# Kernel optimization log

Measured on AMD Instinct MI355X. Metric: run time of the kernel, lower is better.

The kernel has to match this reference:

```python
import jax, jax.numpy as jnp
import numpy as np

B, C, H, W = 64, 2048, 18, 9
INF = 1e9  # larger than any |cost| here (costs are -cosine sims in [-1,1])


def hungarian(cost):
    """Exact O(n^3) Jonker-Volgenant assignment (minimize total cost).
    cost: [n, n] float. Returns int32 [n]: column assigned to each row.
    Matches scipy.optimize.linear_sum_assignment on a square matrix.
    Uses 1-based indexing with a virtual row/column 0 (e-maxx formulation)."""
    n = cost.shape[0]
    costp = jnp.zeros((n + 1, n + 1), cost.dtype).at[1:, 1:].set(cost)
    jr = jnp.arange(n + 1)

    def assign_row(i, carry):
        u, v, p = carry          # u,v: dual potentials; p[j] = row matched to col j
        p = p.at[0].set(i)
        way0 = jnp.zeros(n + 1, jnp.int32)
        minv0 = jnp.full(n + 1, INF, cost.dtype)
        used0 = jnp.zeros(n + 1, bool)

        def cond(st):
            return ~st[6]

        def body(st):
            u, v, way, minv, used, j0, done = st
            used = used.at[j0].set(True)
            i0 = p[j0]
            cur = costp[i0] - u[i0] - v                  # reduced costs of row i0, vectorized over cols
            valid = (~used) & (jr >= 1)
            better = valid & (cur < minv)
            minv = jnp.where(better, cur, minv)
            way = jnp.where(better, j0, way)
            mv = jnp.where(valid, minv, INF)
            j1 = jnp.argmin(mv).astype(jnp.int32)
            delta = mv[j1]
            add = jnp.where(used, delta, jnp.zeros((), cost.dtype))
            u = u.at[p].add(add)                          # used cols have distinct p; unused add 0
            v = v - add
            minv = jnp.where(used, minv, minv - delta)
            return u, v, way, minv, used, j1, p[j1] == 0

        u, v, way, _, _, j0, _ = jax.lax.while_loop(
            cond, body, (u, v, way0, minv0, used0, jnp.int32(0), jnp.array(False)))

        def body2(st):
            j0, p = st
            j1 = way[j0]
            return j1, p.at[j0].set(p[j1])

        _, p = jax.lax.while_loop(lambda st: st[0] != 0, body2, (j0, p))
        return u, v, p

    u = jnp.zeros(n + 1, cost.dtype)
    v = jnp.zeros(n + 1, cost.dtype)
    p = jnp.zeros(n + 1, jnp.int32)
    u, v, p = jax.lax.fori_loop(1, n + 1, assign_row, (u, v, p))
    rowcol = jnp.zeros(n + 1, jnp.int32).at[p[1:]].set(jnp.arange(1, n + 1, dtype=jnp.int32))
    return rowcol[1:] - 1


def compute_mask(feat):
    b, c, h, w = feat.shape
    norms = jnp.linalg.norm(feat, axis=1).reshape(b, h * w)
    norms = norms - norms.min(axis=-1, keepdims=True)
    norms = norms / (norms.max(axis=-1, keepdims=True) + 1e-12)
    return jax.lax.stop_gradient(norms.reshape(b, 1, h, w))


def feature_similarity(fq, fk):
    b, c, h, w = fq.shape
    fq = fq.reshape(b, c, h * w)
    fk = fk.reshape(b, c, h * w)
    # F.normalize(dim=1): x / max(||x||, eps)
    nq = fq / jnp.maximum(jnp.linalg.norm(fq, axis=1, keepdims=True), 1e-12)
    nk = fk / jnp.maximum(jnp.linalg.norm(fk, axis=1, keepdims=True), 1e-12)
    return jnp.einsum('bcn,bcm->bnm', nq, nk)  # [b, n, n]


def setup_inputs() -> dict:
    key = jax.random.key(0)
    k1, k2, k3 = jax.random.split(key, 3)
    feat2d = jax.random.normal(k1, (B, C, H, W), dtype=jnp.float32)
    pos_ind = jax.random.randint(k2, (B,), 0, B, dtype=jnp.int64 if jax.config.jax_enable_x64 else jnp.int32).astype(jnp.int32)
    neg_ind = jax.random.randint(k3, (B,), 0, B, dtype=jnp.int32)
    return {"feat2d": feat2d, "pos_ind": pos_ind, "neg_ind": neg_ind}


def reference(feat2d, pos_ind, neg_ind):
    b, c, h, w = feat2d.shape
    n = h * w
    p = n // 2
    mask = compute_mask(feat2d)                         # [b,1,h,w], detached
    maskTr = mask.reshape(b, 1, n)
    s = jnp.sort(maskTr, axis=2)
    thr = s[:, :, p:p + 1]
    bMask = jnp.where(maskTr < thr, 0.0, 1.0).reshape(mask.shape)  # keep top half
    featMasked = feat2d * jax.lax.stop_gradient(bMask)
    featPos = feat2d[pos_ind]
    simPos = feature_similarity(featMasked, featPos)    # [b, n, n]
    # scipy linear_sum_assignment(sim, maximize=True) == minimize(-sim); indices are constants
    cols = jax.vmap(hungarian)(jax.lax.stop_gradient(-simPos))     # [b, n]
    assigned = jnp.take_along_axis(simPos, cols[:, :, None], axis=2)[..., 0]  # [b, n]
    pos_dis = 1.0 - assigned.sum(axis=-1) / p
    return jnp.mean(pos_dis)
```

## Files before the change

### kernel.cpp

```cpp
#include <hip/hip_runtime.h>
#include <hip/hip_bf16.h>

#define Bn 64
#define Cn 2048
#define Nn 162
#define Pn 81
#define NP 176
#define INFV 1.0e9f
#define BIGI 0x7FFFFFFF
#define RBW 328
#define ARRCAP 700

#define OFF_T    0
#define OFF_P    11534336
#define OFF_QS   (OFF_P + 64*32*192)
#define OFF_KS   (OFF_QS + 64*162)
#define OFF_COST (OFF_KS + 64*162)
#define OFF_PD   (OFF_COST + 64*162*162)

typedef __attribute__((ext_vector_type(8))) short bf16x8;
typedef __attribute__((ext_vector_type(4))) float f32x4;
typedef __attribute__((ext_vector_type(4))) unsigned u32x4;

static __device__ __forceinline__ unsigned short f2bf(float x) {
    unsigned int u = __builtin_bit_cast(unsigned int, x);
    unsigned int r = (u + 0x7fffu + ((u >> 16) & 1u)) >> 16;
    return (unsigned short)r;
}
static __device__ __forceinline__ unsigned short f2h(float x) {
    _Float16 h = (_Float16)x;
    return __builtin_bit_cast(unsigned short, h);
}
static __device__ __forceinline__ float h2f(unsigned short u) {
    return (float)__builtin_bit_cast(_Float16, u);
}
static __device__ __forceinline__ unsigned umin32(unsigned a, unsigned b) { return a < b ? a : b; }
static __device__ __forceinline__ unsigned umax32(unsigned a, unsigned b) { return a > b ? a : b; }
static __device__ __forceinline__ unsigned packnn(float v, int id) {
    float c = fmaxf(v, 0.f);
    return (__builtin_bit_cast(unsigned, c) & 0xFFFFFF00u) | (unsigned)id;
}
static __device__ __forceinline__ float unpacknn(unsigned pk) {
    return __builtin_bit_cast(float, pk & 0xFFFFFF00u);
}
static __device__ __forceinline__ unsigned reduceMin64(unsigned x) {
    int v = (int)x, t;
    t = __builtin_amdgcn_update_dpp(0, v, 0x121, 0xF, 0xF, true); v = (int)umin32((unsigned)v, (unsigned)t);
    t = __builtin_amdgcn_update_dpp(0, v, 0x122, 0xF, 0xF, true); v = (int)umin32((unsigned)v, (unsigned)t);
    t = __builtin_amdgcn_update_dpp(0, v, 0x124, 0xF, 0xF, true); v = (int)umin32((unsigned)v, (unsigned)t);
    t = __builtin_amdgcn_update_dpp(0, v, 0x128, 0xF, 0xF, true); v = (int)umin32((unsigned)v, (unsigned)t);
    unsigned a = (unsigned)__builtin_amdgcn_readlane(v, 0);
    unsigned b = (unsigned)__builtin_amdgcn_readlane(v, 16);
    unsigned c = (unsigned)__builtin_amdgcn_readlane(v, 32);
    unsigned d = (unsigned)__builtin_amdgcn_readlane(v, 48);
    return umin32(umin32(a, b), umin32(c, d));
}
static __device__ __forceinline__ int rlanei(int v, int l) { return __builtin_amdgcn_readlane(v, l); }
static __device__ __forceinline__ float rlanef(float v, int l) {
    return __builtin_bit_cast(float, __builtin_amdgcn_readlane(__builtin_bit_cast(int, v), l));
}
static __device__ __forceinline__ int laneOf(int id) { return id < 128 ? (id >> 1) : (id - 128); }
static __device__ __forceinline__ int slotOf(int id) { return id < 128 ? (id & 1) : 2; }
static __device__ __forceinline__ unsigned long long mask_n(int n) {
    if (n <= 0) return 0ull;
    if (n >= 64) return ~0ull;
    return (1ull << n) - 1ull;
}
#define SEL3(s, a0, a1, a2) ((s) == 0 ? (a0) : ((s) == 1 ? (a1) : (a2)))

__global__ __launch_bounds__(256) void k_tr(const float* __restrict__ feat, float* __restrict__ ws) {
    int x = blockIdx.x;
    int cc = x / 3, ct = x % 3;
    int b = blockIdx.y;
    int tid = threadIdx.x;
    int c2 = tid & 31, pg = tid >> 5;
    __shared__ unsigned Tp[32][65];
    __shared__ float Pp[8][64];
    int gc0 = ct * 64 + 2 * c2;
    bool ok  = (gc0 < Nn);
    bool ok1 = (gc0 + 1 < Nn);
    int gcs = ok ? gc0 : 0;
    const float* fb = feat + ((size_t)b * Cn + (size_t)cc * 64) * Nn;
    float2 fa[4], fc[4];
    #pragma unroll
    for (int it = 0; it < 4; ++it) {
        int p = pg + it * 8;
        fa[it] = *(const float2*)(fb + (size_t)(2 * p) * Nn + gcs);
        fc[it] = *(const float2*)(fb + (size_t)(2 * p + 1) * Nn + gcs);
    }
    float s0 = 0.f, s1 = 0.f;
    #pragma unroll
    for (int it = 0; it < 4; ++it) {
        int p = pg + it * 8;
        float ax = ok  ? fa[it].x : 0.f;
        float ay = ok1 ? fa[it].y : 0.f;
        float cx = ok  ? fc[it].x : 0.f;
        float cy = ok1 ? fc[it].y : 0.f;
        s0 = fmaf(ax, ax, fmaf(cx, cx, s0));
        s1 = fmaf(ay, ay, fmaf(cy, cy, s1));
        Tp[p][2 * c2]     = (unsigned)f2bf(ax) | ((unsigned)f2bf(cx) << 16);
        Tp[p][2 * c2 + 1] = (unsigned)f2bf(ay) | ((unsigned)f2bf(cy) << 16);
    }
    Pp[pg][2 * c2]     = s0;
    Pp[pg][2 * c2 + 1] = s1;
    __syncthreads();
    if (tid < 64) {
        float t = 0.f;
        #pragma unroll
        for (int g = 0; g < 8; ++g) t += Pp[g][tid];
        ws[OFF_P + ((size_t)b * 32 + cc) * 192 + ct * 64 + tid] = t;
    }
    unsigned* ft = (unsigned*)(ws + OFF_T);
    size_t base = ((size_t)(b * 32 + cc) * NP + ct * 64) * 32;
    #pragma unroll
    for (int it = 0; it < 8; ++it) {
        int idx = it * 256 + tid;
        int c = idx >> 5;
        int gcol = ct * 64 + c;
        if (gcol < NP) ft[base + idx] = Tp[idx & 31][c];
    }
}

__global__ __launch_bounds__(256) void k_mm(const int* __restrict__ pos_ind,
                                            float* __restrict__ ws) {
    int wg = blockIdx.x;
    int xcd = wg & 7, kk = wg >> 3;
    int b  = xcd + 8 * (kk / 6);
    int mt = kk % 6;
    int tid = threadIdx.x;
    int lane = tid & 63, w = tid >> 6;
    int q0 = mt * 32;
    int pb = pos_ind[b];
    const u32x4* At = (const u32x4*)((const unsigned short*)(ws + OFF_T) + (size_t)b  * NP * Cn);
    const u32x4* Bt = (const u32x4*)((const unsigned short*)(ws + OFF_T) + (size_t)pb * NP * Cn);
    __shared__ u32x4 As[32 * 16];
    __shared__ u32x4 Bs[176 * 16];

    f32x4 a00 = {0.f, 0.f, 0.f, 0.f}, a01 = a00, a02 = a00, a10 = a00, a11 = a00, a12 = a00;
    const int ct0 = w * 3, ct1 = w * 3 + 1, ct2 = w * 3 + 2;
    const bool has2 = (ct2 < 11);
    const int fr = lane & 15, fq = lane >> 4;

    for (int c0 = 0; c0 < Cn; c0 += 128) {
        int cc0 = c0 >> 6;
        #pragma unroll
        for (int it = 0; it < 2; ++it) {
            int task = it * 256 + tid;
            int r = task >> 4, g = task & 15;
            int rowc = q0 + r; if (rowc > NP - 1) rowc = NP - 1;
            As[r * 16 + (g ^ (r & 15))] = At[((size_t)(cc0 + (g >> 3)) * NP + rowc) * 8 + (g & 7)];
        }
        #pragma unroll
        for (int it = 0; it < 11; ++it) {
            int task = it * 256 + tid;
            int col = task >> 4, g = task & 15;
            Bs[col * 16 + (g ^ (col & 15))] = Bt[((size_t)(cc0 + (g >> 3)) * NP + col) * 8 + (g & 7)];
        }
        __syncthreads();
        #pragma unroll
        for (int ks = 0; ks < 4; ++ks) {
            int gk = ks * 4 + fq;
            bf16x8 af0 = *(const bf16x8*)&As[fr * 16 + (gk ^ fr)];
            bf16x8 af1 = *(const bf16x8*)&As[(16 + fr) * 16 + (gk ^ fr)];
            bf16x8 b0 = *(const bf16x8*)&Bs[(ct0 * 16 + fr) * 16 + (gk ^ fr)];
            bf16x8 b1 = *(const bf16x8*)&Bs[(ct1 * 16 + fr) * 16 + (gk ^ fr)];
            a00 = __builtin_amdgcn_mfma_f32_16x16x32_bf16(af0, b0, a00, 0, 0, 0);
            a01 = __builtin_amdgcn_mfma_f32_16x16x32_bf16(af0, b1, a01, 0, 0, 0);
            a10 = __builtin_amdgcn_mfma_f32_16x16x32_bf16(af1, b0, a10, 0, 0, 0);
            a11 = __builtin_amdgcn_mfma_f32_16x16x32_bf16(af1, b1, a11, 0, 0, 0);
            if (has2) {
                bf16x8 b2 = *(const bf16x8*)&Bs[(ct2 * 16 + fr) * 16 + (gk ^ fr)];
                a02 = __builtin_amdgcn_mfma_f32_16x16x32_bf16(af0, b2, a02, 0, 0, 0);
                a12 = __builtin_amdgcn_mfma_f32_16x16x32_bf16(af1, b2, a12, 0, 0, 0);
            }
        }
        __syncthreads();
    }

    float* simg = ws + OFF_COST + (size_t)b * Nn * Nn;
    int c0_ = ct0 * 16 + fr, c1_ = ct1 * 16 + fr, c2_ = ct2 * 16 + fr;
    #pragma unroll
    for (int j = 0; j < 4; ++j) {
        int r0 = q0 + fq * 4 + j;
        int r1 = r0 + 16;
        if (r0 < Nn) {
            if (c0_ < Nn) simg[(size_t)r0 * Nn + c0_] = a00[j];
            if (c1_ < Nn) simg[(size_t)r0 * Nn + c1_] = a01[j];
            if (has2 && c2_ < Nn) simg[(size_t)r0 * Nn + c2_] = a02[j];
        }
        if (r1 < Nn) {
            if (c0_ < Nn) simg[(size_t)r1 * Nn + c0_] = a10[j];
            if (c1_ < Nn) simg[(size_t)r1 * Nn + c1_] = a11[j];
            if (has2 && c2_ < Nn) simg[(size_t)r1 * Nn + c2_] = a12[j];
        }
    }
}

__global__ __launch_bounds__(256) void k_hung(float* __restrict__ ws) {
    const int b = blockIdx.x;
    const int tid = threadIdx.x;
    const int lane = tid & 63, wv = tid >> 6;
    __shared__ unsigned short Cw[(Nn * RBW) / 2 + 32];
    __shared__ int rowBest[Nn + 1];
    __shared__ float Ulds[Nn + 1];
    __shared__ float dvA[192];
    __shared__ float pcm[4][192];
    __shared__ int   pim[4][192];
    __shared__ short rowIdxL[Nn];
    __shared__ float qsL[192];
    __shared__ float ksL[192];
    const float* cg = ws + OFF_COST + (size_t)b * Nn * Nn;

    const bool v2ok = (lane < Nn - 128);
    const int id0 = 2 * lane, id1 = 2 * lane + 1, id2 = 128 + lane;
    const int a32 = 4 * lane;
    const int a16 = 256 + 2 * lane;

    if (tid <= Nn) { rowBest[tid] = BIGI; Ulds[tid] = 0.f; }
    if (tid < 192) dvA[tid] = 0.f;

    float* arrS = &pcm[0][0];
    float* thrP = &pcm[1][0];
    float normv = 0.f, mvalv = 0.f;
    if (tid < Nn) {
        float s = 0.f;
        #pragma unroll
        for (int ch = 0; ch < 32; ++ch) s += ws[OFF_P + ((size_t)b * 32 + ch) * 192 + tid];
        normv = sqrtf(s);
        arrS[tid] = normv;
    }
    __syncthreads();
    {
        float mn = INFV, mx = -INFV;
        for (int k = 0; k < Nn; ++k) { float v = arrS[k]; mn = fminf(mn, v); mx = fmaxf(mx, v); }
        if (tid < Nn) mvalv = (normv - mn) / (mx - mn + 1e-12f);
    }
    __syncthreads();
    if (tid < Nn) arrS[tid] = mvalv;
    __syncthreads();
    if (tid < Nn) {
        int cl = 0, ce = 0, ceb = 0;
        for (int k = 0; k < Nn; ++k) {
            float v = arrS[k];
            cl  += (v <  mvalv);
            ce  += (v == mvalv);
            ceb += (v == mvalv && k < tid);
        }
        if (cl <= Pn && (cl + ce) > Pn && ceb == 0) thrP[0] = mvalv;
    }
    if (tid < 192) { qsL[tid] = 0.f; ksL[tid] = 0.f; }
    __syncthreads();
    if (tid < Nn) {
        float inv = 1.f / fmaxf(normv, 1e-12f);
        ksL[tid] = inv;
        qsL[tid] = (mvalv < thrP[0]) ? 0.f : inv;
    }
    __syncthreads();

    const float ks0f = ksL[id0];
    const float ks1f = ksL[id1];
    const float ks2f = v2ok ? ksL[id2] : 0.f;

    float aq0 = qsL[lane];
    float aq1 = qsL[64 + lane];
    float aq2 = v2ok ? qsL[128 + lane] : 0.f;
    unsigned long long act0 = __ballot(aq0 != 0.f);
    unsigned long long act1 = __ballot(aq1 != 0.f);
    unsigned long long act2 = __ballot(v2ok && aq2 != 0.f);
    int n0 = __popcll(act0), n1 = __popcll(act1), n2 = __popcll(act2);
    const int nact = n0 + n1 + n2;
    if (nact == 0) { if (tid == 0) ws[OFF_PD + b] = 1.f; return; }

    if (wv == 0) {
        unsigned long long lt = (1ull << lane) - 1;
        if ((act0 >> lane) & 1) rowIdxL[__popcll(act0 & lt)] = (short)lane;
        if ((act1 >> lane) & 1) rowIdxL[n0 + __popcll(act1 & lt)] = (short)(64 + lane);
        if (v2ok && ((act2 >> lane) & 1)) rowIdxL[n0 + n1 + __popcll(act2 & lt)] = (short)(128 + lane);
    }
    __syncthreads();

    for (int k = wv; k < nact; k += 4) {
        int orig = rowIdxL[k];
        float qsr = qsL[orig];
        float2 f2 = *(const float2*)(cg + (size_t)orig * Nn + 2 * lane);
        unsigned pk = (unsigned)f2h(-(f2.x * qsr * ks0f))
                    | ((unsigned)f2h(-(f2.y * qsr * ks1f)) << 16);
        *(unsigned*)((char*)Cw + k * RBW + a32) = pk;
        if (v2ok) *(unsigned short*)((char*)Cw + k * RBW + a16) =
            f2h(-(cg[(size_t)orig * Nn + 128 + lane] * qsr * ks2f));
    }
    __syncthreads();

    float cm0 = INFV, cm1 = INFV, cm2 = INFV; int im0 = 0, im1 = 0, im2 = 0;
    for (int k = wv; k < nact; k += 4) {
        unsigned pr = *(const unsigned*)((const char*)Cw + k * RBW + a32);
        float c0 = h2f((unsigned short)pr);
        float c1 = h2f((unsigned short)(pr >> 16));
        float c2 = h2f(*(const unsigned short*)((const char*)Cw + k * RBW + a16));
        if (c0 < cm0) { cm0 = c0; im0 = k + 1; }
        if (c1 < cm1) { cm1 = c1; im1 = k + 1; }
        if (v2ok && c2 < cm2) { cm2 = c2; im2 = k + 1; }
    }
    pcm[wv][id0] = cm0; pim[wv][id0] = im0;
    pcm[wv][id1] = cm1; pim[wv][id1] = im1;
    if (v2ok) { pcm[wv][id2] = cm2; pim[wv][id2] = im2; }
    __syncthreads();

    cm0 = INFV; im0 = 0; cm1 = INFV; im1 = 0; cm2 = INFV; im2 = 0;
    #pragma unroll
    for (int ww = 0; ww < 4; ++ww) {
        float c; int im;
        c = pcm[ww][id0]; im = pim[ww][id0];
        if (im > 0 && (im0 == 0 || c < cm0 || (c == cm0 && im < im0))) { cm0 = c; im0 = im; }
        c = pcm[ww][id1]; im = pim[ww][id1];
        if (im > 0 && (im1 == 0 || c < cm1 || (c == cm1 && im < im1))) { cm1 = c; im1 = im; }
        if (v2ok) {
            c = pcm[ww][id2]; im = pim[ww][id2];
            if (im > 0 && (im2 == 0 || c < cm2 || (c == cm2 && im < im2))) { cm2 = c; im2 = im; }
        }
    }
    if (wv == 0) {
        if (im0 > 0) atomicMin(&rowBest[im0], id0);
        if (im1 > 0) atomicMin(&rowBest[im1], id1);
        if (v2ok && im2 > 0) atomicMin(&rowBest[im2], id2);
    }
    __syncthreads();

    float v0 = cm0, v1 = cm1, v2 = v2ok ? cm2 : 0.f;
    int Pa0 = (im0 > 0 && rowBest[im0] == id0) ? im0 : 0;
    int Pa1 = (im1 > 0 && rowBest[im1] == id1) ? im1 : 0;
    int Pa2 = (v2ok && im2 > 0 && rowBest[im2] == id2) ? im2 : 0;

    unsigned long long cb0 = __ballot(lane + 1 <= nact && rowBest[lane + 1] != BIGI);
    unsigned long long cb1 = __ballot(lane + 65 <= nact && rowBest[lane + 65] != BIGI);
    unsigned long long cb2 = __ballot(lane + 129 <= nact && rowBest[lane + 129] != BIGI);
    unsigned long long fr0 = mask_n(nact)       & ~cb0;
    unsigned long long fr1 = mask_n(nact - 64)  & ~cb1;
    unsigned long long fr2 = mask_n(nact - 128) & ~cb2;

    for (int k = wv; k < nact; k += 4) {
        int j1c = rowBest[k + 1];
        if (j1c == BIGI) continue;
        int roff = k * RBW;
        unsigned pr = *(const unsigned*)((const char*)Cw + roff + a32);
        float r0 = h2f((unsigned short)pr) - v0;
        float r1 = h2f((unsigned short)(pr >> 16)) - v1;
        float r2 = h2f(*(const unsigned short*)((const char*)Cw + roff + a16)) - v2;
        unsigned p0 = (id0 == j1c) ? 0xFFFFFFFFu : packnn(r0, id0);
        unsigned p1 = (id1 == j1c) ? 0xFFFFFFFFu : packnn(r1, id1);
        unsigned p2 = (v2ok && id2 != j1c) ? packnn(r2, id2) : 0xFFFFFFFFu;
        unsigned pk = reduceMin64(umin32(p0, umin32(p1, p2)));
        float min2 = unpacknn(pk);
        if (lane == 0) { dvA[j1c] = min2; Ulds[k + 1] = min2; }
    }
    __syncthreads();
    if (wv != 0) return;

    float ur0, ur1, ur2;
    v0 -= dvA[id0]; ur0 = dvA[id0];
    v1 -= dvA[id1]; ur1 = dvA[id1];
    if (v2ok) { v2 -= dvA[id2]; ur2 = dvA[id2]; } else ur2 = 0.f;

    float minv0 = INFV, minv1 = INFV, minv2 = INFV;
    int way0 = 255, way1 = 255, way2 = 255;
    bool used0 = false, used1 = false, used2 = false;

    unsigned long long nx0 = 0, nx1 = 0, nx2 = 0;
    int arrIt = 0;
    for (int pass = 0; pass < 2; ++pass) {
        while ((fr0 | fr1 | fr2) != 0 && arrIt < ARRCAP) {
            ++arrIt;
            int i;
            if (fr0)      { int t = __builtin_ctzll(fr0); i = t + 1;   fr0 &= fr0 - 1; }
            else if (fr1) { int t = __builtin_ctzll(fr1); i = t + 65;  fr1 &= fr1 - 1; }
            else          { int t = __builtin_ctzll(fr2); i = t + 129; fr2 &= fr2 - 1; }
            int roff = (i - 1) * RBW;
            unsigned pr = *(const unsigned*)((const char*)Cw + roff + a32);
            float r0 = h2f((unsigned short)pr) - v0;
            float r1 = h2f((unsigned short)(pr >> 16)) - v1;
            float r2 = h2f(*(const unsigned short*)((const char*)Cw + roff + a16)) - v2;
            unsigned p0 = packnn(r0, id0);
            unsigned p1 = packnn(r1, id1);
            unsigned p2 = v2ok ? packnn(r2, id2) : 0xFFFFFFFFu;
            unsigned lmin = umin32(p0, umin32(p1, p2));
            unsigned lmed = umin32(umax32(p0, p1), umax32(umin32(p0, p1), p2));
            unsigned M1 = reduceMin64(lmin);
            unsigned M2 = reduceMin64(lmin == M1 ? lmed : lmin);
            int j1 = (int)(M1 & 0xFFu), j2 = (int)(M2 & 0xFFu);
            int l1 = laneOf(j1), s1 = slotOf(j1);
            int l2 = laneOf(j2), s2 = slotOf(j2);
            float umin_e = rlanef(SEL3(s1, r0, r1, r2), l1);
            float usub_e = rlanef(SEL3(s2, r0, r1, r2), l2);
            int iA = rlanei(SEL3(s1, Pa0, Pa1, Pa2), l1);
            int iB = rlanei(SEL3(s2, Pa0, Pa1, Pa2), l2);
            if (usub_e < umin_e) {
                int tj = j1; j1 = j2; j2 = tj;
                int tl = l1; l1 = l2; l2 = tl;
                int ts = s1; s1 = s2; s2 = ts;
                float tv = umin_e; umin_e = usub_e; usub_e = tv;
                int ti = iA; iA = iB; iB = ti;
            }
            bool strict = (umin_e < usub_e);
            int jt, idisp;
            float ua = usub_e;
            if (strict) {
                float d = usub_e - umin_e;
                if (lane == l1) { if (s1 == 0) v0 -= d; else if (s1 == 1) v1 -= d; else v2 -= d; }
                jt = j1; idisp = iA;
            } else if (iA > 0) {
                jt = j2; idisp = iB;
            } else {
                jt = j1; idisp = 0;
            }
            int lt = laneOf(jt), st = slotOf(jt);
            if (lane == lt) {
                if (st == 0)      { Pa0 = i; ur0 = ua; }
                else if (st == 1) { Pa1 = i; ur1 = ua; }
                else              { Pa2 = i; ur2 = ua; }
            }
            if (lane == 0) Ulds[i] = ua;
            if (idisp > 0) {
                if (strict) {
                    if (idisp <= 64)       fr0 |= 1ull << (idisp - 1);
                    else if (idisp <= 128) fr1 |= 1ull << (idisp - 65);
                    else                   fr2 |= 1ull << (idisp - 129);
                } else {
                    if (idisp <= 64)       nx0 |= 1ull << (idisp - 1);
                    else if (idisp <= 128) nx1 |= 1ull << (idisp - 65);
                    else                   nx2 |= 1ull << (idisp - 129);
                }
            }
        }
        fr0 |= nx0; fr1 |= nx1; fr2 |= nx2;
        nx0 = nx1 = nx2 = 0;
    }

    while ((fr0 | fr1 | fr2) != 0) {
        int i;
        if (fr0)      { int t = __builtin_ctzll(fr0); i = t + 1;   fr0 &= fr0 - 1; }
        else if (fr1) { int t = __builtin_ctzll(fr1); i = t + 65;  fr1 &= fr1 - 1; }
        else          { int t = __builtin_ctzll(fr2); i = t + 129; fr2 &= fr2 - 1; }
        float u_root = Ulds[i];
        minv0 = minv1 = minv2 = INFV;
        way0 = way1 = way2 = 255;
        used0 = used1 = used2 = false;
        {
            int roff = (i - 1) * RBW;
            unsigned pr = *(const unsigned*)((const char*)Cw + roff + a32);
            float c0 = h2f((unsigned short)pr);
            float c1 = h2f((unsigned short)(pr >> 16));
            float c2 = h2f(*(const unsigned short*)((const char*)Cw + roff + a16));
            minv0 = c0 - (u_root + v0);
            minv1 = c1 - (u_root + v1);
            minv2 = v2ok ? (c2 - (u_root + v2)) : INFV;
        }
        int jend = -1;
        for (int it = 0; it < Nn + 2; ++it) {
            unsigned q0p = used0 ? 0xFFFFFFFFu : packnn(minv0, id0);
            unsigned q1p = used1 ? 0xFFFFFFFFu : packnn(minv1, id1);
            unsigned q2p = (v2ok && !used2) ? packnn(minv2, id2) : 0xFFFFFFFFu;
            unsigned pk = reduceMin64(umin32(q0p, umin32(q1p, q2p)));
            int j1 = (int)(pk & 0xFFu);
            float delta = unpacknn(pk);
            int l1 = laneOf(j1), s1 = slotOf(j1);
            int i1 = rlanei(SEL3(s1, Pa0, Pa1, Pa2), l1);
            float u1 = rlanef(SEL3(s1, ur0, ur1, ur2), l1);
            u_root += delta;
            v0 = used0 ? v0 - delta : v0;  ur0 = used0 ? ur0 + delta : ur0;  minv0 = used0 ? minv0 : minv0 - delta;
            v1 = used1 ? v1 - delta : v1;  ur1 = used1 ? ur1 + delta : ur1;  minv1 = used1 ? minv1 : minv1 - delta;
            v2 = used2 ? v2 - delta : v2;  ur2 = used2 ? ur2 + delta : ur2;  minv2 = used2 ? minv2 : minv2 - delta;
            bool hit = (lane == l1);
            if (s1 == 0) used0 |= hit; else if (s1 == 1) used1 |= hit; else used2 |= hit;
            if (i1 == 0) { jend = j1; break; }
            int roff = (i1 - 1) * RBW;
            unsigned pr = *(const unsigned*)((const char*)Cw + roff + a32);
            float c0 = h2f((unsigned short)pr);
            float c1 = h2f((unsigned short)(pr >> 16));
            float c2 = h2f(*(const unsigned short*)((const char*)Cw + roff + a16));
            float n0_ = c0 - (u1 + v0), n1_ = c1 - (u1 + v1), n2_ = c2 - (u1 + v2);
            if (!used0 && n0_ < minv0) { minv0 = n0_; way0 = j1; }
            if (!used1 && n1_ < minv1) { minv1 = n1_; way1 = j1; }
            if (v2ok && !used2 && n2_ < minv2) { minv2 = n2_; way2 = j1; }
        }
        int j = jend;
        while (j >= 0) {
            int l = laneOf(j), s = slotOf(j);
            int w = rlanei(SEL3(s, way0, way1, way2), l);
            int pnew; float unew;
            if (w == 255) { pnew = i; unew = u_root; }
            else {
                int lw = laneOf(w), sw = slotOf(w);
                pnew = rlanei(SEL3(sw, Pa0, Pa1, Pa2), lw);
                unew = rlanef(SEL3(sw, ur0, ur1, ur2), lw);
            }
            if (lane == l) {
                if (s == 0)      { Pa0 = pnew; ur0 = unew; }
                else if (s == 1) { Pa1 = pnew; ur1 = unew; }
                else             { Pa2 = pnew; ur2 = unew; }
            }
            j = (w == 255) ? -1 : w;
        }
    }

    float tot = 0.f;
    if (Pa0 > 0) { int orig = rowIdxL[Pa0 - 1]; tot += cg[(size_t)orig * Nn + id0] * qsL[orig] * ks0f; }
    if (Pa1 > 0) { int orig = rowIdxL[Pa1 - 1]; tot += cg[(size_t)orig * Nn + id1] * qsL[orig] * ks1f; }
    if (v2ok && Pa2 > 0) { int orig = rowIdxL[Pa2 - 1]; tot += cg[(size_t)orig * Nn + id2] * qsL[orig] * ks2f; }
    #pragma unroll
    for (int off = 32; off; off >>= 1) tot += __shfl_xor(tot, off);
    if (lane == 0) ws[OFF_PD + b] = 1.f - tot * (1.f / (float)Pn);
}

__global__ void k_final(const float* __restrict__ ws, float* __restrict__ out) {
    float v = ws[OFF_PD + threadIdx.x];
    #pragma unroll
    for (int off = 32; off; off >>= 1) v += __shfl_xor(v, off);
    if (threadIdx.x == 0) out[0] = v * (1.f / 64.f);
}

extern "C" void kernel_launch(void* const* d_in, const int* in_sizes, int n_in,
                              void* d_out, int out_size, void* d_ws, size_t ws_size,
                              hipStream_t stream) {
    const float* feat = (const float*)d_in[0];
    const int*   pos  = (const int*)d_in[1];
    float* ws  = (float*)d_ws;
    float* out = (float*)d_out;
    k_tr   <<<dim3(96, 64), 256, 0, stream>>>(feat, ws);
    k_mm   <<<384, 256, 0, stream>>>(pos, ws);
    k_hung <<<64, 256, 0, stream>>>(ws);
    k_final<<<1, 64, 0, stream>>>(ws, out);
}
```

Baseline: 102.4 us.

## Restructure transpose kernel to load full 64-channel slab with float4 coalesced reads

The transpose/convert kernel now gives each block all 162 spatial columns for a 64-channel slab instead of splitting them into three 64-column tiles, which cuts the grid from 96x64 to 32x64 blocks. Input is read contiguously with float4 loads, packed to bf16 pairs in shared memory, then re-paired across channels and written out, with padding columns zeroed explicitly. Per-column squared norms are computed by separate strided global re-reads from the first 162 threads. The goal is fewer blocks and wider, coalesced global reads. In exchange the input is read twice, shared-memory indexing needs integer divides, and the unpacking on the write side is more complex.

```diff
diff --git a/kernel.cpp b/kernel.cpp
--- a/kernel.cpp
+++ b/kernel.cpp
@@ -69,55 +69,64 @@
 #define SEL3(s, a0, a1, a2) ((s) == 0 ? (a0) : ((s) == 1 ? (a1) : (a2)))
 
 __global__ __launch_bounds__(256) void k_tr(const float* __restrict__ feat, float* __restrict__ ws) {
-    int x = blockIdx.x;
-    int cc = x / 3, ct = x % 3;
-    int b = blockIdx.y;
+    int cc = blockIdx.x;
+    int b  = blockIdx.y;
     int tid = threadIdx.x;
-    int c2 = tid & 31, pg = tid >> 5;
-    __shared__ unsigned Tp[32][65];
-    __shared__ float Pp[8][64];
-    int gc0 = ct * 64 + 2 * c2;
-    bool ok  = (gc0 < Nn);
-    bool ok1 = (gc0 + 1 < Nn);
-    int gcs = ok ? gc0 : 0;
+    __shared__ unsigned Ld[64][83];
     const float* fb = feat + ((size_t)b * Cn + (size_t)cc * 64) * Nn;
-    float2 fa[4], fc[4];
+
     #pragma unroll
-    for (int it = 0; it < 4; ++it) {
-        int p = pg + it * 8;
-        fa[it] = *(const float2*)(fb + (size_t)(2 * p) * Nn + gcs);
-        fc[it] = *(const float2*)(fb + (size_t)(2 * p + 1) * Nn + gcs);
-    }
-    float s0 = 0.f, s1 = 0.f;
+    for (int it = 0; it < 10; ++it) {
+        int k = it * 256 + tid;
+        float4 v = *(const float4*)(fb + 4 * k);
+        int qa = 4 * k;
+        int qb = qa + 2;
+        int cha = (unsigned)qa / 162u, cola = qa - cha * 162;
+        int chb = (unsigned)qb / 162u, colb = qb - chb * 162;
+        Ld[cha][cola >> 1] = (unsigned)f2bf(v.x) | ((unsigned)f2bf(v.y) << 16);
+        Ld[chb][colb >> 1] = (unsigned)f2bf(v.z) | ((unsigned)f2bf(v.w) << 16);
+    }
+    if (tid < 32) {
+        int k = 2560 + tid;
+        float4 v = *(const float4*)(fb + 4 * k);
+        int qa = 4 * k, qb = qa + 2;
+        int cha = (unsigned)qa / 162u, cola = qa - cha * 162;
+        int chb = (unsigned)qb / 162u, colb = qb - chb * 162;
+        Ld[cha][cola >> 1] = (unsigned)f2bf(v.x) | ((unsigned)f2bf(v.y) << 16);
+        Ld[chb][colb >> 1] = (unsigned)f2bf(v.z) | ((unsigned)f2bf(v.w) << 16);
+    }
+
+    if (tid < Nn) {
+        float s0 = 0.f, s1 = 0.f, s2 = 0.f, s3 = 0.f;
+        #pragma unroll 4
+        for (int ch = 0; ch < 64; ch += 4) {
+            float a0 = fb[(size_t)ch * Nn + tid];
+            float a1 = fb[(size_t)(ch + 1) * Nn + tid];
+            float a2 = fb[(size_t)(ch + 2) * Nn + tid];
+            float a3 = fb[(size_t)(ch + 3) * Nn + tid];
+            s0 = fmaf(a0, a0, s0);
+            s1 = fmaf(a1, a1, s1);
+            s2 = fmaf(a2, a2, s2);
+            s3 = fmaf(a3, a3, s3);
+        }
+        ws[OFF_P + ((size_t)b * 32 + cc) * 192 + tid] = (s0 + s1) + (s2 + s3);
+    }
+    __syncthreads();
+
+    unsigned* ft = (unsigned*)(ws + OFF_T);
+    size_t base = (size_t)(b * 32 + cc) * NP * 32;
     #pragma unroll
-    for (int it = 0; it < 4; ++it) {
-        int p = pg + it * 8;
-        float ax = ok  ? fa[it].x : 0.f;
-        float ay = ok1 ? fa[it].y : 0.f;
-        float cx = ok  ? fc[it].x : 0.f;
-        float cy = ok1 ? fc[it].y : 0.f;
-        s0 = fmaf(ax, ax, fmaf(cx, cx, s0));
-        s1 = fmaf(ay, ay, fmaf(cy, cy, s1));
-        Tp[p][2 * c2]     = (unsigned)f2bf(ax) | ((unsigned)f2bf(cx) << 16);
-        Tp[p][2 * c2 + 1] = (unsigned)f2bf(ay) | ((unsigned)f2bf(cy) << 16);
-    }
-    Pp[pg][2 * c2]     = s0;
-    Pp[pg][2 * c2 + 1] = s1;
-    __syncthreads();
-    if (tid < 64) {
-        float t = 0.f;
-        #pragma unroll
-        for (int g = 0; g < 8; ++g) t += Pp[g][tid];
-        ws[OFF_P + ((size_t)b * 32 + cc) * 192 + ct * 64 + tid] = t;
-    }
-    unsigned* ft = (unsigned*)(ws + OFF_T);
-    size_t base = ((size_t)(b * 32 + cc) * NP + ct * 64) * 32;
-    #pragma unroll
-    for (int it = 0; it < 8; ++it) {
+    for (int it = 0; it < 22; ++it) {
         int idx = it * 256 + tid;
-        int c = idx >> 5;
-        int gcol = ct * 64 + c;
-        if (gcol < NP) ft[base + idx] = Tp[idx & 31][c];
+        int p = idx & 31, gcol = idx >> 5;
+        unsigned outw = 0u;
+        if (gcol < Nn) {
+            unsigned w0 = Ld[2 * p][gcol >> 1];
+            unsigned w1 = Ld[2 * p + 1][gcol >> 1];
+            if (gcol & 1) { outw = (w0 >> 16) | (w1 & 0xFFFF0000u); }
+            else          { outw = (w0 & 0xFFFFu) | (w1 << 16); }
+        }
+        ft[base + idx] = outw;
     }
 }
 
@@ -525,7 +534,7 @@
     const int*   pos  = (const int*)d_in[1];
     float* ws  = (float*)d_ws;
     float* out = (float*)d_out;
-    k_tr   <<<dim3(96, 64), 256, 0, stream>>>(feat, ws);
+    k_tr   <<<dim3(32, 64), 256, 0, stream>>>(feat, ws);
     k_mm   <<<384, 256, 0, stream>>>(pos, ws);
     k_hung <<<64, 256, 0, stream>>>(ws);
     k_final<<<1, 64, 0, stream>>>(ws, out);
```

Measured after the change: 107.2 us. 4.7% more time.
